# Kernel tuning notes

Measured on AMD Instinct MI355X. Metric: run time of the kernel, lower is better.

## Reference

```python
import jax, jax.numpy as jnp
import numpy as np

B, S, H, D = 1, 8192, 16, 128
DIM = H * D
POSITION = S - 1  # decode at the last cache slot -> attends over full 8K cache
W_STD = 0.02      # realistic init scale so attention logits are well-conditioned


def setup_inputs() -> dict:
    key = jax.random.key(0)
    ks = jax.random.split(key, 7)
    x = jax.random.normal(ks[0], (B, 1, DIM), dtype=jnp.float32)
    k_cache = jax.random.normal(ks[1], (B, S, H, D), dtype=jnp.float32)
    v_cache = jax.random.normal(ks[2], (B, S, H, D), dtype=jnp.float32)
    w_q = jax.random.normal(ks[3], (DIM, DIM), dtype=jnp.float32) * W_STD
    w_k = jax.random.normal(ks[4], (DIM, DIM), dtype=jnp.float32) * W_STD
    w_v = jax.random.normal(ks[5], (DIM, DIM), dtype=jnp.float32) * W_STD
    w_o = jax.random.normal(ks[6], (DIM, DIM), dtype=jnp.float32) * W_STD
    return {"x": x, "k_cache": k_cache, "v_cache": v_cache,
            "w_q": w_q, "w_k": w_k, "w_v": w_v, "w_o": w_o,
            "position": POSITION}


def reference(x, k_cache, v_cache, w_q, w_k, w_v, w_o, position):
    # decode_step: single token x -> q/k/v projections (torch Linear: y = x @ W.T)
    b = x.shape[0]
    h, d = k_cache.shape[2], k_cache.shape[3]
    dim = x.shape[-1]
    q = (x @ w_q.T).reshape(b, 1, h, d)      # [B,1,H,D]
    k_new = (x @ w_k.T).reshape(b, 1, h, d)
    v_new = (x @ w_v.T).reshape(b, 1, h, d)
    # append current token's K/V into the cache at `position` (static Python int)
    k_cache = k_cache.at[:, position:position + 1].set(k_new)
    v_cache = v_cache.at[:, position:position + 1].set(v_new)
    k_past = k_cache[:, :position + 1]       # [B,K,H,D], K = position+1
    v_past = v_cache[:, :position + 1]
    scale = 1.0 / np.sqrt(d).astype(np.float32)
    # single-query causal decode: the query at `position` may attend to all
    # cached keys [0..position], so no mask is needed.
    scores = jnp.einsum('bqhd,bkhd->bhqk', q, k_past) * scale  # [B,H,1,K]
    attn = jax.nn.softmax(scores, axis=-1)
    out = jnp.einsum('bhqk,bkhd->bqhd', attn, v_past).reshape(b, 1, dim)
    return out @ w_o.T                        # [B,1,dim]
```

## Files before the change

kernel.cpp:

```cpp
#include <hip/hip_runtime.h>
#include <math.h>

namespace {
constexpr int kDim = 2048;
constexpr int kH = 16;
constexpr int kD = 128;
constexpr int kS = 8192;
constexpr int kChunk = 64;
constexpr int kNChunk = kS / kChunk;
constexpr float kScale = 0.08838834764831843f;
}

__global__ __launch_bounds__(256) void qkv_gemv(
    const float* __restrict__ x, const float* __restrict__ wq,
    const float* __restrict__ wk, const float* __restrict__ wv,
    float* __restrict__ qkv)
{
    const int wid  = (blockIdx.x << 2) | ((int)threadIdx.x >> 6);
    const int lane = threadIdx.x & 63;
    const float* W;
    int r = wid;
    if (r < kDim)            { W = wq; }
    else if (r < 2 * kDim)   { W = wk; r -= kDim; }
    else                     { W = wv; r -= 2 * kDim; }
    const float4* wrow = reinterpret_cast<const float4*>(W + (size_t)r * kDim);
    const float4* x4   = reinterpret_cast<const float4*>(x);
    float4 wr[8], xv[8];
#pragma unroll
    for (int k = 0; k < 8; ++k) wr[k] = wrow[(k << 6) + lane];
#pragma unroll
    for (int k = 0; k < 8; ++k) xv[k] = x4[(k << 6) + lane];
    float acc = 0.f;
#pragma unroll
    for (int k = 0; k < 8; ++k)
        acc += wr[k].x * xv[k].x + wr[k].y * xv[k].y
             + wr[k].z * xv[k].z + wr[k].w * xv[k].w;
#pragma unroll
    for (int off = 32; off; off >>= 1) acc += __shfl_xor(acc, off, 64);
    if (lane == 0) qkv[wid] = acc;
}

__global__ __launch_bounds__(256) void attn_fused(
    const float* __restrict__ k_cache, const float* __restrict__ v_cache,
    const float* __restrict__ qkv, const int* __restrict__ pos_p,
    float* __restrict__ part)
{
    const int h     = blockIdx.x >> 7;
    const int chunk = blockIdx.x & (kNChunk - 1);
    const int wave  = threadIdx.x >> 6;
    const int lane  = threadIdx.x & 63;
    const int half  = lane >> 5;
    const int l32   = lane & 31;
    const int pos   = pos_p[0];
    const int s0    = chunk * kChunk;
    const int kb    = s0 + wave * 16;

    __shared__ float  sm[4], sl[4];
    __shared__ float4 sacc[4][32];

    const float4* knew4 = reinterpret_cast<const float4*>(qkv + kDim + h * kD);
    const float4* vnew4 = reinterpret_cast<const float4*>(qkv + 2 * kDim + h * kD);
    const float4* kp0 = reinterpret_cast<const float4*>(k_cache)
                        + (size_t)(kb + half) * (kH * kD / 4) + h * (kD / 4) + l32;
    const float4* vp0 = reinterpret_cast<const float4*>(v_cache)
                        + (size_t)(kb + half) * (kH * kD / 4) + h * (kD / 4) + l32;
    const bool tail = (kb + 16 > pos);

    const float4 q4 = reinterpret_cast<const float4*>(qkv + h * kD)[l32];

    float p[8];
    {
        float4 kv[8];
        if (!tail) {
#pragma unroll
            for (int j = 0; j < 8; ++j) kv[j] = kp0[(size_t)j * 1024];
        } else {
#pragma unroll
            for (int j = 0; j < 8; ++j) {
                const int key = kb + 2 * j + half;
                kv[j] = (key == pos) ? knew4[l32] : kp0[(size_t)j * 1024];
            }
        }
#pragma unroll
        for (int j = 0; j < 8; ++j)
            p[j] = kv[j].x * q4.x + kv[j].y * q4.y + kv[j].z * q4.z + kv[j].w * q4.w;
    }

    float4 vv[8];
    if (!tail) {
#pragma unroll
        for (int j = 0; j < 8; ++j) vv[j] = vp0[(size_t)j * 1024];
    } else {
#pragma unroll
        for (int j = 0; j < 8; ++j) {
            const int key = kb + 2 * j + half;
            vv[j] = (key == pos) ? vnew4[l32] : vp0[(size_t)j * 1024];
        }
    }

#pragma unroll
    for (int mask = 1; mask <= 16; mask <<= 1) {
#pragma unroll
        for (int i = 0; i < 8; ++i)
            p[i] += __shfl_xor(p[i], mask, 32);
    }
    if (!tail) {
#pragma unroll
        for (int i = 0; i < 8; ++i) p[i] *= kScale;
    } else {
#pragma unroll
        for (int i = 0; i < 8; ++i) {
            const int key = kb + 2 * i + half;
            p[i] = (key <= pos) ? p[i] * kScale : -INFINITY;
        }
    }

    float mw = p[0];
#pragma unroll
    for (int i = 1; i < 8; ++i) mw = fmaxf(mw, p[i]);
    mw = fmaxf(mw, __shfl_xor(mw, 32, 64));
    float e[8];
    float es = 0.f;
#pragma unroll
    for (int i = 0; i < 8; ++i) {
        e[i] = (p[i] > -INFINITY) ? __expf(p[i] - mw) : 0.f;
        es += e[i];
    }
    const float lw = es + __shfl_xor(es, 32, 64);

    float4 acc = make_float4(0.f, 0.f, 0.f, 0.f);
#pragma unroll
    for (int j = 0; j < 8; ++j) {
        acc.x += e[j] * vv[j].x;
        acc.y += e[j] * vv[j].y;
        acc.z += e[j] * vv[j].z;
        acc.w += e[j] * vv[j].w;
    }
    acc.x += __shfl_xor(acc.x, 32, 64);
    acc.y += __shfl_xor(acc.y, 32, 64);
    acc.z += __shfl_xor(acc.z, 32, 64);
    acc.w += __shfl_xor(acc.w, 32, 64);

    if (half == 0) sacc[wave][l32] = acc;
    if (lane == 0) { sm[wave] = mw; sl[wave] = lw; }
    __syncthreads();

    if (wave == 0 && lane < 32) {
        const float M = fmaxf(fmaxf(sm[0], sm[1]), fmaxf(sm[2], sm[3]));
        float L = 0.f;
        float4 A = make_float4(0.f, 0.f, 0.f, 0.f);
#pragma unroll
        for (int w = 0; w < 4; ++w) {
            if (sl[w] > 0.f) {
                const float f = __expf(sm[w] - M);
                const float4 a = sacc[w][l32];
                L   += sl[w] * f;
                A.x += a.x * f; A.y += a.y * f; A.z += a.z * f; A.w += a.w * f;
            }
        }
        float* pp = part + (size_t)(h * kNChunk + chunk) * (kD + 2);
        reinterpret_cast<float4*>(pp)[l32] = A;
        if (l32 == 0) { pp[kD] = M; pp[kD + 1] = L; }
    }
}

__global__ __launch_bounds__(128) void combine_partials(
    const float* __restrict__ part, float* __restrict__ o_out)
{
    const int h    = blockIdx.x;
    const int t    = threadIdx.x;
    const int wave = t >> 6;
    const int lane = t & 63;
    __shared__ float wred[2], wsum[2], f_lds[kNChunk];

    const float* pp = part + (size_t)(h * kNChunk + t) * (kD + 2);
    const float mc = pp[kD];
    const float lc = pp[kD + 1];

    float mg = mc;
#pragma unroll
    for (int m = 32; m; m >>= 1) mg = fmaxf(mg, __shfl_xor(mg, m, 64));
    if (lane == 0) wred[wave] = mg;
    __syncthreads();
    const float Mg = fmaxf(wred[0], wred[1]);

    const float f = (lc > 0.f) ? __expf(mc - Mg) : 0.f;
    f_lds[t] = f;
    float lf = lc * f;
#pragma unroll
    for (int m = 32; m; m >>= 1) lf += __shfl_xor(lf, m, 64);
    if (lane == 0) wsum[wave] = lf;
    __syncthreads();
    const float Lg = wsum[0] + wsum[1];

    float O = 0.f;
    const float* base = part + (size_t)h * kNChunk * (kD + 2) + t;
#pragma unroll 8
    for (int c = 0; c < kNChunk; ++c)
        O += base[(size_t)c * (kD + 2)] * f_lds[c];
    o_out[h * kD + t] = O / Lg;
}

__global__ __launch_bounds__(256) void out_gemv(
    const float* __restrict__ o, const float* __restrict__ wo,
    float* __restrict__ out)
{
    const int wid  = (blockIdx.x << 2) | ((int)threadIdx.x >> 6);
    const int lane = threadIdx.x & 63;
    const float4* wrow = reinterpret_cast<const float4*>(wo + (size_t)wid * kDim);
    const float4* x4   = reinterpret_cast<const float4*>(o);
    float4 wr[8], xv[8];
#pragma unroll
    for (int k = 0; k < 8; ++k) wr[k] = wrow[(k << 6) + lane];
#pragma unroll
    for (int k = 0; k < 8; ++k) xv[k] = x4[(k << 6) + lane];
    float acc = 0.f;
#pragma unroll
    for (int k = 0; k < 8; ++k)
        acc += wr[k].x * xv[k].x + wr[k].y * xv[k].y
             + wr[k].z * xv[k].z + wr[k].w * xv[k].w;
#pragma unroll
    for (int off = 32; off; off >>= 1) acc += __shfl_xor(acc, off, 64);
    if (lane == 0) out[wid] = acc;
}

extern "C" void kernel_launch(void* const* d_in, const int* in_sizes, int n_in,
                              void* d_out, int out_size, void* d_ws, size_t ws_size,
                              hipStream_t stream)
{
    const float* x       = (const float*)d_in[0];
    const float* k_cache = (const float*)d_in[1];
    const float* v_cache = (const float*)d_in[2];
    const float* wq      = (const float*)d_in[3];
    const float* wk      = (const float*)d_in[4];
    const float* wv      = (const float*)d_in[5];
    const float* wo      = (const float*)d_in[6];
    const int*   pos     = (const int*)d_in[7];
    float* out = (float*)d_out;

    float* ws    = (float*)d_ws;
    float* qkv   = ws;
    float* part  = qkv + 3 * kDim;
    float* o_out = part + kH * kNChunk * (kD + 2);

    qkv_gemv<<<3 * kDim / 4, 256, 0, stream>>>(x, wq, wk, wv, qkv);
    attn_fused<<<kH * kNChunk, 256, 0, stream>>>(k_cache, v_cache, qkv, pos, part);
    combine_partials<<<kH, 128, 0, stream>>>(part, o_out);
    out_gemv<<<kDim / 4, 256, 0, stream>>>(o_out, wo, out);
}
```

Before: 51.94 us.

## Restructure attention so each block processes all heads for a 16-key chunk

The attention kernel now assigns each block a 16-row sequence chunk spanning all 16 heads, so it reads whole contiguous 8 KB K/V rows instead of strided per-head slices. Scores go through LDS for a per-head softmax, V loads are software-pipelined with explicit waitcnt fences, and the max/sum values are written to a separate float2 array. The change trades more partials (512 chunks per head) for contiguous memory access. That makes combine_partials read four times as many partial vectors, which adds reduction traffic.

```diff
diff --git a/kernel.cpp b/kernel.cpp
--- a/kernel.cpp
+++ b/kernel.cpp
@@ -6,10 +6,15 @@
 constexpr int kH = 16;
 constexpr int kD = 128;
 constexpr int kS = 8192;
-constexpr int kChunk = 64;
-constexpr int kNChunk = kS / kChunk;
+constexpr int kChunk = 16;
+constexpr int kNC = kS / kChunk;
 constexpr float kScale = 0.08838834764831843f;
 }
+
+#define BATCH_FENCE() do { \
+    asm volatile("s_waitcnt vmcnt(0)" ::: "memory"); \
+    __builtin_amdgcn_sched_barrier(0); \
+} while (0)
 
 __global__ __launch_bounds__(256) void qkv_gemv(
     const float* __restrict__ x, const float* __restrict__ wq,
@@ -43,150 +48,154 @@
 __global__ __launch_bounds__(256) void attn_fused(
     const float* __restrict__ k_cache, const float* __restrict__ v_cache,
     const float* __restrict__ qkv, const int* __restrict__ pos_p,
-    float* __restrict__ part)
-{
-    const int h     = blockIdx.x >> 7;
-    const int chunk = blockIdx.x & (kNChunk - 1);
+    float* __restrict__ part, float2* __restrict__ ml)
+{
+    const int chunk = blockIdx.x;
     const int wave  = threadIdx.x >> 6;
     const int lane  = threadIdx.x & 63;
     const int half  = lane >> 5;
     const int l32   = lane & 31;
     const int pos   = pos_p[0];
-    const int s0    = chunk * kChunk;
-    const int kb    = s0 + wave * 16;
-
-    __shared__ float  sm[4], sl[4];
-    __shared__ float4 sacc[4][32];
-
-    const float4* knew4 = reinterpret_cast<const float4*>(qkv + kDim + h * kD);
-    const float4* vnew4 = reinterpret_cast<const float4*>(qkv + 2 * kDim + h * kD);
-    const float4* kp0 = reinterpret_cast<const float4*>(k_cache)
-                        + (size_t)(kb + half) * (kH * kD / 4) + h * (kD / 4) + l32;
-    const float4* vp0 = reinterpret_cast<const float4*>(v_cache)
-                        + (size_t)(kb + half) * (kH * kD / 4) + h * (kD / 4) + l32;
-    const bool tail = (kb + 16 > pos);
-
-    const float4 q4 = reinterpret_cast<const float4*>(qkv + h * kD)[l32];
-
-    float p[8];
-    {
+    const int kb0   = chunk * kChunk;
+
+    __shared__ float s_lds[kH][kChunk];
+
+    const float4* kc4   = reinterpret_cast<const float4*>(k_cache);
+    const float4* vc4   = reinterpret_cast<const float4*>(v_cache);
+    const float4* qkv4  = reinterpret_cast<const float4*>(qkv);
+    const float4* knew4 = qkv4 + 512;
+    const float4* vnew4 = qkv4 + 1024;
+
+    float4 qreg[8];
+#pragma unroll
+    for (int g = 0; g < 8; ++g)
+        qreg[g] = qkv4[(2 * g + half) * 32 + l32];
+
+#pragma unroll
+    for (int i = 0; i < 4; ++i) {
+        const int rl  = wave * 4 + i;
+        const int row = kb0 + rl;
+        const float4* kr = (row == pos) ? knew4 : (kc4 + (size_t)row * 512);
         float4 kv[8];
-        if (!tail) {
-#pragma unroll
-            for (int j = 0; j < 8; ++j) kv[j] = kp0[(size_t)j * 1024];
-        } else {
+#pragma unroll
+        for (int g = 0; g < 8; ++g) kv[g] = kr[g * 64 + lane];
+        BATCH_FENCE();
+        float p[8];
+#pragma unroll
+        for (int g = 0; g < 8; ++g)
+            p[g] = kv[g].x * qreg[g].x + kv[g].y * qreg[g].y
+                 + kv[g].z * qreg[g].z + kv[g].w * qreg[g].w;
+#pragma unroll
+        for (int mask = 1; mask <= 16; mask <<= 1) {
+#pragma unroll
+            for (int g = 0; g < 8; ++g) p[g] += __shfl_xor(p[g], mask, 32);
+        }
+        if (l32 == 0) {
+            const bool valid = (row <= pos);
+#pragma unroll
+            for (int g = 0; g < 8; ++g)
+                s_lds[2 * g + half][rl] = valid ? p[g] * kScale : -INFINITY;
+        }
+    }
+
+    const int g2a = 2 * wave;
+    float4 vv[8];
+#pragma unroll
+    for (int j = 0; j < 8; ++j) {
+        const int row = kb0 + (j >> 1);
+        const int g2  = g2a + (j & 1);
+        const float4* vr = (row == pos) ? vnew4 : (vc4 + (size_t)row * 512);
+        vv[j] = vr[g2 * 64 + lane];
+    }
+
+    __syncthreads();
+
+#pragma unroll
+    for (int gi = 0; gi < 2; ++gi) {
+        const int h = 2 * (g2a + gi) + half;
+        float s_r = (l32 < kChunk) ? s_lds[h][l32] : -INFINITY;
+        float mh = s_r;
+#pragma unroll
+        for (int mask = 1; mask <= 16; mask <<= 1)
+            mh = fmaxf(mh, __shfl_xor(mh, mask, 32));
+        const float eh = (s_r > -INFINITY) ? __expf(s_r - mh) : 0.f;
+        float lh = eh;
+#pragma unroll
+        for (int mask = 1; mask <= 16; mask <<= 1)
+            lh += __shfl_xor(lh, mask, 32);
+        if (l32 < kChunk) s_lds[h][l32] = eh;
+        if (l32 == 0) ml[h * kNC + chunk] = make_float2(mh, lh);
+    }
+
+    float4 acc0 = make_float4(0.f, 0.f, 0.f, 0.f);
+    float4 acc1 = make_float4(0.f, 0.f, 0.f, 0.f);
+#pragma unroll
+    for (int b = 0; b < 4; ++b) {
+        BATCH_FENCE();
+        float4 cur[8];
+#pragma unroll
+        for (int j = 0; j < 8; ++j) cur[j] = vv[j];
+        if (b < 3) {
 #pragma unroll
             for (int j = 0; j < 8; ++j) {
-                const int key = kb + 2 * j + half;
-                kv[j] = (key == pos) ? knew4[l32] : kp0[(size_t)j * 1024];
+                const int row = kb0 + 4 * (b + 1) + (j >> 1);
+                const int g2  = g2a + (j & 1);
+                const float4* vr = (row == pos) ? vnew4 : (vc4 + (size_t)row * 512);
+                vv[j] = vr[g2 * 64 + lane];
             }
         }
 #pragma unroll
-        for (int j = 0; j < 8; ++j)
-            p[j] = kv[j].x * q4.x + kv[j].y * q4.y + kv[j].z * q4.z + kv[j].w * q4.w;
-    }
-
-    float4 vv[8];
-    if (!tail) {
-#pragma unroll
-        for (int j = 0; j < 8; ++j) vv[j] = vp0[(size_t)j * 1024];
-    } else {
-#pragma unroll
         for (int j = 0; j < 8; ++j) {
-            const int key = kb + 2 * j + half;
-            vv[j] = (key == pos) ? vnew4[l32] : vp0[(size_t)j * 1024];
-        }
-    }
-
-#pragma unroll
-    for (int mask = 1; mask <= 16; mask <<= 1) {
-#pragma unroll
-        for (int i = 0; i < 8; ++i)
-            p[i] += __shfl_xor(p[i], mask, 32);
-    }
-    if (!tail) {
-#pragma unroll
-        for (int i = 0; i < 8; ++i) p[i] *= kScale;
-    } else {
-#pragma unroll
-        for (int i = 0; i < 8; ++i) {
-            const int key = kb + 2 * i + half;
-            p[i] = (key <= pos) ? p[i] * kScale : -INFINITY;
-        }
-    }
-
-    float mw = p[0];
-#pragma unroll
-    for (int i = 1; i < 8; ++i) mw = fmaxf(mw, p[i]);
-    mw = fmaxf(mw, __shfl_xor(mw, 32, 64));
-    float e[8];
-    float es = 0.f;
-#pragma unroll
-    for (int i = 0; i < 8; ++i) {
-        e[i] = (p[i] > -INFINITY) ? __expf(p[i] - mw) : 0.f;
-        es += e[i];
-    }
-    const float lw = es + __shfl_xor(es, 32, 64);
-
-    float4 acc = make_float4(0.f, 0.f, 0.f, 0.f);
-#pragma unroll
-    for (int j = 0; j < 8; ++j) {
-        acc.x += e[j] * vv[j].x;
-        acc.y += e[j] * vv[j].y;
-        acc.z += e[j] * vv[j].z;
-        acc.w += e[j] * vv[j].w;
-    }
-    acc.x += __shfl_xor(acc.x, 32, 64);
-    acc.y += __shfl_xor(acc.y, 32, 64);
-    acc.z += __shfl_xor(acc.z, 32, 64);
-    acc.w += __shfl_xor(acc.w, 32, 64);
-
-    if (half == 0) sacc[wave][l32] = acc;
-    if (lane == 0) { sm[wave] = mw; sl[wave] = lw; }
-    __syncthreads();
-
-    if (wave == 0 && lane < 32) {
-        const float M = fmaxf(fmaxf(sm[0], sm[1]), fmaxf(sm[2], sm[3]));
-        float L = 0.f;
-        float4 A = make_float4(0.f, 0.f, 0.f, 0.f);
-#pragma unroll
-        for (int w = 0; w < 4; ++w) {
-            if (sl[w] > 0.f) {
-                const float f = __expf(sm[w] - M);
-                const float4 a = sacc[w][l32];
-                L   += sl[w] * f;
-                A.x += a.x * f; A.y += a.y * f; A.z += a.z * f; A.w += a.w * f;
+            const int rl = 4 * b + (j >> 1);
+            const int h  = 2 * (g2a + (j & 1)) + half;
+            const float e = s_lds[h][rl];
+            if ((j & 1) == 0) {
+                acc0.x += e * cur[j].x; acc0.y += e * cur[j].y;
+                acc0.z += e * cur[j].z; acc0.w += e * cur[j].w;
+            } else {
+                acc1.x += e * cur[j].x; acc1.y += e * cur[j].y;
+                acc1.z += e * cur[j].z; acc1.w += e * cur[j].w;
             }
         }
-        float* pp = part + (size_t)(h * kNChunk + chunk) * (kD + 2);
-        reinterpret_cast<float4*>(pp)[l32] = A;
-        if (l32 == 0) { pp[kD] = M; pp[kD + 1] = L; }
-    }
+    }
+
+    float4* part4 = reinterpret_cast<float4*>(part);
+    const int h0 = 2 * g2a + half;
+    const int h1 = 2 * (g2a + 1) + half;
+    part4[((size_t)h0 * kNC + chunk) * 32 + l32] = acc0;
+    part4[((size_t)h1 * kNC + chunk) * 32 + l32] = acc1;
 }
 
 __global__ __launch_bounds__(128) void combine_partials(
-    const float* __restrict__ part, float* __restrict__ o_out)
+    const float* __restrict__ part, const float2* __restrict__ ml,
+    float* __restrict__ o_out)
 {
     const int h    = blockIdx.x;
     const int t    = threadIdx.x;
     const int wave = t >> 6;
     const int lane = t & 63;
-    __shared__ float wred[2], wsum[2], f_lds[kNChunk];
-
-    const float* pp = part + (size_t)(h * kNChunk + t) * (kD + 2);
-    const float mc = pp[kD];
-    const float lc = pp[kD + 1];
-
-    float mg = mc;
-#pragma unroll
-    for (int m = 32; m; m >>= 1) mg = fmaxf(mg, __shfl_xor(mg, m, 64));
-    if (lane == 0) wred[wave] = mg;
+    __shared__ float wred[2], wsum[2], f_lds[kNC];
+
+    float2 mlv[4];
+    float mloc = -INFINITY;
+#pragma unroll
+    for (int k = 0; k < 4; ++k) {
+        mlv[k] = ml[h * kNC + t + 128 * k];
+        mloc = fmaxf(mloc, mlv[k].x);
+    }
+#pragma unroll
+    for (int m = 32; m; m >>= 1) mloc = fmaxf(mloc, __shfl_xor(mloc, m, 64));
+    if (lane == 0) wred[wave] = mloc;
     __syncthreads();
     const float Mg = fmaxf(wred[0], wred[1]);
 
-    const float f = (lc > 0.f) ? __expf(mc - Mg) : 0.f;
-    f_lds[t] = f;
-    float lf = lc * f;
+    float lf = 0.f;
+#pragma unroll
+    for (int k = 0; k < 4; ++k) {
+        const float f = (mlv[k].y > 0.f) ? __expf(mlv[k].x - Mg) : 0.f;
+        f_lds[t + 128 * k] = f;
+        lf += mlv[k].y * f;
+    }
 #pragma unroll
     for (int m = 32; m; m >>= 1) lf += __shfl_xor(lf, m, 64);
     if (lane == 0) wsum[wave] = lf;
@@ -194,10 +203,10 @@
     const float Lg = wsum[0] + wsum[1];
 
     float O = 0.f;
-    const float* base = part + (size_t)h * kNChunk * (kD + 2) + t;
+    const float* base = part + (size_t)h * kNC * kD + t;
 #pragma unroll 8
-    for (int c = 0; c < kNChunk; ++c)
-        O += base[(size_t)c * (kD + 2)] * f_lds[c];
+    for (int c = 0; c < kNC; ++c)
+        O += f_lds[c] * base[(size_t)c * kD];
     o_out[h * kD + t] = O / Lg;
 }
 
@@ -238,13 +247,14 @@
     const int*   pos     = (const int*)d_in[7];
     float* out = (float*)d_out;
 
-    float* ws    = (float*)d_ws;
-    float* qkv   = ws;
-    float* part  = qkv + 3 * kDim;
-    float* o_out = part + kH * kNChunk * (kD + 2);
+    float*  ws    = (float*)d_ws;
+    float*  qkv   = ws;
+    float*  part  = qkv + 3 * kDim;
+    float2* ml    = (float2*)(part + (size_t)kH * kNC * kD);
+    float*  o_out = (float*)(ml + kH * kNC);
 
     qkv_gemv<<<3 * kDim / 4, 256, 0, stream>>>(x, wq, wk, wv, qkv);
-    attn_fused<<<kH * kNChunk, 256, 0, stream>>>(k_cache, v_cache, qkv, pos, part);
-    combine_partials<<<kH, 128, 0, stream>>>(part, o_out);
+    attn_fused<<<kNC, 256, 0, stream>>>(k_cache, v_cache, qkv, pos, part, ml);
+    combine_partials<<<kH, 128, 0, stream>>>(part, ml, o_out);
     out_gemv<<<kDim / 4, 256, 0, stream>>>(o_out, wo, out);
 }
```

Result: slower. 56.77 us (+9.3%).
